# Performance work log

Measured on AMD Instinct MI355X. Metric: run time of the kernel, lower is better.

## Reference

```python
import jax, jax.numpy as jnp
import numpy as np

WS = 9
PAD = WS // 2  # 4


def _unfold(x, H, W):
    # x: [N,C,H,W] -> [N,C,81,H,W], reflect-padded 9x9 windows,
    # tap order (row-major over kernel) matching torch F.unfold.
    xp = jnp.pad(x, ((0, 0), (0, 0), (PAD, PAD), (PAD, PAD)), mode='reflect')
    return jnp.stack(
        [xp[:, :, i:i + H, j:j + W] for i in range(WS) for j in range(WS)],
        axis=2,
    )


def _bilinear_align_corners(x, H, W):
    # torch F.interpolate(mode='bilinear', align_corners=True)
    N, C, h, w = x.shape
    ys = jnp.linspace(0.0, h - 1.0, H)
    xs = jnp.linspace(0.0, w - 1.0, W)
    y0 = jnp.floor(ys).astype(jnp.int32)
    x0 = jnp.floor(xs).astype(jnp.int32)
    y1 = jnp.minimum(y0 + 1, h - 1)
    x1 = jnp.minimum(x0 + 1, w - 1)
    wy = (ys - y0)[:, None]   # [H,1]
    wx = (xs - x0)[None, :]   # [1,W]
    g = lambda yi, xi: x[:, :, yi, :][:, :, :, xi]
    top = g(y0, x0) * (1.0 - wx) + g(y0, x1) * wx
    bot = g(y1, x0) * (1.0 - wx) + g(y1, x1) * wx
    return top * (1.0 - wy) + bot * wy


def setup_inputs() -> dict:
    key = jax.random.key(0)
    ks = jax.random.split(key, 6)
    N, H, W = 4, 128, 128
    return {
        'delta': jax.random.normal(ks[0], (N, 64, H, W), jnp.float32),
        'out': jax.random.normal(ks[1], (N, 2, H // 2, W // 2), jnp.float32),
        'ab_logits': jax.random.normal(ks[2], (N, 81, H * W), jnp.float32),
        'w1': jax.random.normal(ks[3], (16, 64), jnp.float32) * 0.125,
        'b1': jnp.zeros((16,), jnp.float32),
        'w2': jax.random.normal(ks[4], (16, 64), jnp.float32) * 0.125,
        'b2': jnp.zeros((16,), jnp.float32),
        'gamma_d': jnp.ones((), jnp.float32),
        'gamma_s': jnp.ones((), jnp.float32),
    }


def reference(delta, out, ab_logits, w1, b1, w2, b2, gamma_d, gamma_s):
    N, C, H, W = delta.shape
    # 1x1 convs
    f1 = jnp.einsum('nchw,oc->nohw', delta, w1) + b1[None, :, None, None]
    f2 = jnp.einsum('nchw,oc->nohw', delta, w2) + b2[None, :, None, None]
    # windowed squared-distance correlation
    f2_unf = _unfold(f2, H, W).reshape(N, 16, WS * WS, H * W)
    d_center = f1.reshape(N, 16, 1, H * W)
    delta_logits = -jnp.sum((d_center - f2_unf) ** 2, axis=1)  # [N,81,HW]
    attn = jax.nn.softmax(gamma_d * delta_logits + gamma_s * ab_logits, axis=1)
    # weighted local aggregation of (detached, upsampled) out
    out_up = _bilinear_align_corners(jax.lax.stop_gradient(out), H, W)
    out_unf = _unfold(out_up, H, W).reshape(N, 2, WS * WS, H * W)
    out_refine = jnp.sum(out_unf * attn[:, None], axis=2)  # [N,2,HW]
    return out_refine.reshape(N, 2, H, W)
```

## Files before the change

### kernel.cpp

```cpp
#include <hip/hip_runtime.h>

#define HW   16384
#define NPIX 65536

typedef _Float16 f16x2 __attribute__((ext_vector_type(2)));

#if __has_builtin(__builtin_amdgcn_fdot2)
#define DOT2(a, b, c) __builtin_amdgcn_fdot2((a), (b), (c), false)
#else
__device__ __forceinline__ float dot2_fb(f16x2 a, f16x2 b, float c) {
    return fmaf((float)a.x, (float)b.x, fmaf((float)a.y, (float)b.y, c));
}
#define DOT2(a, b, c) dot2_fb((a), (b), (c))
#endif

#if __has_builtin(__builtin_amdgcn_exp2f)
#define EXP2F(x) __builtin_amdgcn_exp2f(x)
#else
#define EXP2F(x) exp2f(x)
#endif

__device__ __forceinline__ unsigned packh2(float a, float b) {
    f16x2 h; h.x = (_Float16)a; h.y = (_Float16)b;
    return __builtin_bit_cast(unsigned, h);
}
__device__ __forceinline__ f16x2 bch(unsigned u) {
    return __builtin_bit_cast(f16x2, u);
}

__global__ __launch_bounds__(256) void pass1_kernel(
    const float* __restrict__ delta, const float* __restrict__ outlo,
    const float* __restrict__ w1, const float* __restrict__ b1,
    const float* __restrict__ w2, const float* __restrict__ b2,
    uint4* __restrict__ f1p4, uint4* __restrict__ f2p4, float2* __restrict__ recp)
{
    const int g = blockIdx.x * 256 + threadIdx.x;
    const int n = g >> 14;
    const int p = g & (HW - 1);

    float acc1[16], acc2[16];
#pragma unroll
    for (int o = 0; o < 16; ++o) { acc1[o] = b1[o]; acc2[o] = b2[o]; }

    const float* db = delta + (size_t)n * 64 * HW + p;
#pragma unroll
    for (int cc = 0; cc < 4; ++cc) {
        float d[16];
#pragma unroll
        for (int j = 0; j < 16; ++j) d[j] = db[(cc * 16 + j) * HW];
#pragma unroll
        for (int o = 0; o < 16; ++o) {
            const float* w1r = w1 + o * 64 + cc * 16;
            const float* w2r = w2 + o * 64 + cc * 16;
#pragma unroll
            for (int j = 0; j < 16; ++j) {
                acc1[o] = fmaf(w1r[j], d[j], acc1[o]);
                acc2[o] = fmaf(w2r[j], d[j], acc2[o]);
            }
        }
    }

    float f2sq = 0.f;
#pragma unroll
    for (int o = 0; o < 16; ++o) f2sq = fmaf(acc2[o], acc2[o], f2sq);

    uint4 q;
    q.x = packh2(acc1[0], acc1[1]);  q.y = packh2(acc1[2], acc1[3]);
    q.z = packh2(acc1[4], acc1[5]);  q.w = packh2(acc1[6], acc1[7]);
    f1p4[g] = q;
    q.x = packh2(acc1[8], acc1[9]);  q.y = packh2(acc1[10], acc1[11]);
    q.z = packh2(acc1[12], acc1[13]);q.w = packh2(acc1[14], acc1[15]);
    f1p4[NPIX + g] = q;
    q.x = packh2(acc2[0], acc2[1]);  q.y = packh2(acc2[2], acc2[3]);
    q.z = packh2(acc2[4], acc2[5]);  q.w = packh2(acc2[6], acc2[7]);
    f2p4[g] = q;
    q.x = packh2(acc2[8], acc2[9]);  q.y = packh2(acc2[10], acc2[11]);
    q.z = packh2(acc2[12], acc2[13]);q.w = packh2(acc2[14], acc2[15]);
    f2p4[NPIX + g] = q;

    const int y = p >> 7, x = p & 127;
    const float ys = (float)(y * 63) / 127.0f;
    const float xs = (float)(x * 63) / 127.0f;
    const int iy0 = (int)ys, ix0 = (int)xs;
    const float fy = ys - (float)iy0, fx = xs - (float)ix0;
    const int iy1 = min(iy0 + 1, 63), ix1 = min(ix0 + 1, 63);
    const float* ob = outlo + n * 2 * 4096;
    float o01[2];
#pragma unroll
    for (int cc = 0; cc < 2; ++cc) {
        const float* oc = ob + cc * 4096;
        const float v00 = oc[iy0*64+ix0], v01 = oc[iy0*64+ix1];
        const float v10 = oc[iy1*64+ix0], v11 = oc[iy1*64+ix1];
        const float top = v00 + fx * (v01 - v00);
        const float bot = v10 + fx * (v11 - v10);
        o01[cc] = top + fy * (bot - top);
    }
    float2 rc;
    rc.x = __builtin_bit_cast(float, packh2(o01[0], o01[1]));
    rc.y = f2sq;
    recp[g] = rc;
}

__global__ __launch_bounds__(128) void pass2_kernel(
    const uint4* __restrict__ f1p4, const uint4* __restrict__ f2p4,
    const float2* __restrict__ recp, const float* __restrict__ ab,
    const float* __restrict__ gdp, const float* __restrict__ gsp,
    float* __restrict__ outp)
{
    __shared__ unsigned sh[24 * 25 * 12];

    const int t = threadIdx.x;
    const int n = blockIdx.z;
    const int bx = blockIdx.x * 16, by = blockIdx.y * 16;

#pragma unroll
    for (int s = 0; s < 5; ++s) {
        const int idx = t + s * 128;
        if (idx < 576) {
            const int hy = idx / 24, hx = idx - hy * 24;
            int gy = by - 4 + hy; gy = gy < 0 ? -gy : (gy > 127 ? 254 - gy : gy);
            int gx = bx - 4 + hx; gx = gx < 0 ? -gx : (gx > 127 ? 254 - gx : gx);
            const int g = n * HW + gy * 128 + gx;
            const uint4  q0 = f2p4[g];
            const uint4  q1 = f2p4[NPIX + g];
            const float2 rc = recp[g];
            const int b = (hy * 25 + hx) * 12;
            *(uint4*)&sh[b]     = q0;
            *(uint4*)&sh[b + 4] = q1;
            *(float2*)&sh[b + 8] = rc;
        }
    }
    __syncthreads();

    const float gd = gdp[0], gs = gsp[0];
    const float L2E = 1.44269504088896f;
    const int tx2 = t & 7, ty = t >> 3;
    const int x0 = bx + tx2 * 2, y = by + ty;
    const int p0 = y * 128 + x0;
    const int g0 = n * HW + p0;

    f16x2 f1a[8], f1b[8];
    {
        const uint4 A0 = f1p4[g0],     A1 = f1p4[NPIX + g0];
        const uint4 B0 = f1p4[g0 + 1], B1 = f1p4[NPIX + g0 + 1];
        f1a[0]=bch(A0.x); f1a[1]=bch(A0.y); f1a[2]=bch(A0.z); f1a[3]=bch(A0.w);
        f1a[4]=bch(A1.x); f1a[5]=bch(A1.y); f1a[6]=bch(A1.z); f1a[7]=bch(A1.w);
        f1b[0]=bch(B0.x); f1b[1]=bch(B0.y); f1b[2]=bch(B0.z); f1b[3]=bch(B0.w);
        f1b[4]=bch(B1.x); f1b[5]=bch(B1.y); f1b[6]=bch(B1.z); f1b[7]=bch(B1.w);
    }
    float f1sqa = 0.f, f1sqb = 0.f;
#pragma unroll
    for (int k = 0; k < 8; ++k) {
        f1sqa = DOT2(f1a[k], f1a[k], f1sqa);
        f1sqb = DOT2(f1b[k], f1b[k], f1sqb);
    }
    const float g2  = 2.0f * gd * L2E;
    const float mg  = -gd * L2E;
    const float gsl = gs * L2E;
    const float c0a = mg * f1sqa;
    const float c0b = mg * f1sqb;

    const float2* abp = (const float2*)ab + (size_t)n * 81 * (HW / 2) + (p0 >> 1);

    float2 cur[9], nxt[9];
#pragma unroll
    for (int j = 0; j < 9; ++j) cur[j] = abp[(size_t)j * (HW / 2)];

    float s0 = 0.f, x00 = 0.f, x01 = 0.f;
    float s1 = 0.f, x10 = 0.f, x11 = 0.f;

    for (int dy = 0; dy < 9; ++dy) {
        const int nr = (dy < 8) ? dy + 1 : 8;
#pragma unroll
        for (int j = 0; j < 9; ++j) nxt[j] = abp[(size_t)(nr * 9 + j) * (HW / 2)];

        const int rowb = ((ty + dy) * 25 + tx2 * 2) * 12;
#pragma unroll
        for (int dxc = 0; dxc < 10; ++dxc) {
            const int b = rowb + dxc * 12;
            const uint4  q0 = *(const uint4*)&sh[b];
            const uint4  q1 = *(const uint4*)&sh[b + 4];
            const float2 rc = *(const float2*)&sh[b + 8];
            f16x2 f2v[8];
            f2v[0]=bch(q0.x); f2v[1]=bch(q0.y); f2v[2]=bch(q0.z); f2v[3]=bch(q0.w);
            f2v[4]=bch(q1.x); f2v[5]=bch(q1.y); f2v[6]=bch(q1.z); f2v[7]=bch(q1.w);
            const f16x2 oh = bch(__builtin_bit_cast(unsigned, rc.x));
            const float o0f = (float)oh.x, o1f = (float)oh.y;
            const float f2s = rc.y;
            if (dxc <= 8) {
                float dt = 0.f;
#pragma unroll
                for (int k = 0; k < 8; ++k) dt = DOT2(f1a[k], f2v[k], dt);
                float e = fmaf(g2, dt, c0a);
                e = fmaf(mg, f2s, e);
                e = fmaf(gsl, cur[dxc].x, e);
                const float w = EXP2F(e);
                s0 += w; x00 = fmaf(w, o0f, x00); x01 = fmaf(w, o1f, x01);
            }
            if (dxc >= 1) {
                float dt = 0.f;
#pragma unroll
                for (int k = 0; k < 8; ++k) dt = DOT2(f1b[k], f2v[k], dt);
                float e = fmaf(g2, dt, c0b);
                e = fmaf(mg, f2s, e);
                e = fmaf(gsl, cur[dxc - 1].y, e);
                const float w = EXP2F(e);
                s1 += w; x10 = fmaf(w, o0f, x10); x11 = fmaf(w, o1f, x11);
            }
        }
#pragma unroll
        for (int j = 0; j < 9; ++j) cur[j] = nxt[j];
    }

    const float i0 = 1.0f / s0, i1 = 1.0f / s1;
    float2* o0p = (float2*)(outp + (size_t)(n * 2 + 0) * HW + p0);
    float2* o1p = (float2*)(outp + (size_t)(n * 2 + 1) * HW + p0);
    *o0p = make_float2(x00 * i0, x10 * i1);
    *o1p = make_float2(x01 * i0, x11 * i1);
}

extern "C" void kernel_launch(void* const* d_in, const int* in_sizes, int n_in,
                              void* d_out, int out_size, void* d_ws, size_t ws_size,
                              hipStream_t stream) {
    const float* delta = (const float*)d_in[0];
    const float* outlo = (const float*)d_in[1];
    const float* ab    = (const float*)d_in[2];
    const float* w1    = (const float*)d_in[3];
    const float* b1    = (const float*)d_in[4];
    const float* w2    = (const float*)d_in[5];
    const float* b2    = (const float*)d_in[6];
    const float* gd    = (const float*)d_in[7];
    const float* gs    = (const float*)d_in[8];
    float* outp = (float*)d_out;

    uint4*  f1p4 = (uint4*)d_ws;
    uint4*  f2p4 = f1p4 + (size_t)2 * NPIX;
    float2* recp = (float2*)(f2p4 + (size_t)2 * NPIX);

    pass1_kernel<<<dim3(256), dim3(256), 0, stream>>>(delta, outlo, w1, b1, w2, b2,
                                                      f1p4, f2p4, recp);
    pass2_kernel<<<dim3(8, 8, 4), dim3(128), 0, stream>>>(f1p4, f2p4, recp, ab,
                                                          gd, gs, outp);
}
```

Before: 116.6 us.

## Split pass1 by conv and pass2 window rows across waves with LDS reduction

Pass1 now launches two blocks per pixel group, one for each 1x1 conv, which doubles parallelism but reads delta twice. Pass2 switches to 8x16 tiles with 256 threads, where each wave handles a subset of window rows for two vertically adjacent pixels. Partial softmax sums are reduced through shared memory. The aim is more waves for the 256-CU GPU and coalesced per-pixel ab loads, at the cost of extra LDS traffic and a second barrier.

```diff
diff --git a/kernel.cpp b/kernel.cpp
--- a/kernel.cpp
+++ b/kernel.cpp
@@ -34,115 +34,111 @@
     const float* __restrict__ w2, const float* __restrict__ b2,
     uint4* __restrict__ f1p4, uint4* __restrict__ f2p4, float2* __restrict__ recp)
 {
+    const int m = blockIdx.y;
     const int g = blockIdx.x * 256 + threadIdx.x;
     const int n = g >> 14;
     const int p = g & (HW - 1);
 
-    float acc1[16], acc2[16];
-#pragma unroll
-    for (int o = 0; o < 16; ++o) { acc1[o] = b1[o]; acc2[o] = b2[o]; }
-
+    const float* __restrict__ wm = m ? w2 : w1;
+    const float* __restrict__ bm = m ? b2 : b1;
+
+    float d[64];
     const float* db = delta + (size_t)n * 64 * HW + p;
 #pragma unroll
-    for (int cc = 0; cc < 4; ++cc) {
-        float d[16];
-#pragma unroll
-        for (int j = 0; j < 16; ++j) d[j] = db[(cc * 16 + j) * HW];
-#pragma unroll
-        for (int o = 0; o < 16; ++o) {
-            const float* w1r = w1 + o * 64 + cc * 16;
-            const float* w2r = w2 + o * 64 + cc * 16;
-#pragma unroll
-            for (int j = 0; j < 16; ++j) {
-                acc1[o] = fmaf(w1r[j], d[j], acc1[o]);
-                acc2[o] = fmaf(w2r[j], d[j], acc2[o]);
-            }
-        }
-    }
-
-    float f2sq = 0.f;
-#pragma unroll
-    for (int o = 0; o < 16; ++o) f2sq = fmaf(acc2[o], acc2[o], f2sq);
-
+    for (int c = 0; c < 64; ++c) d[c] = db[(size_t)c * HW];
+
+    float acc[16];
+#pragma unroll
+    for (int o = 0; o < 16; ++o) {
+        float a = bm[o];
+        const float* wr = wm + o * 64;
+#pragma unroll
+        for (int c = 0; c < 64; ++c) a = fmaf(wr[c], d[c], a);
+        acc[o] = a;
+    }
+
+    uint4* dst = m ? f2p4 : f1p4;
     uint4 q;
-    q.x = packh2(acc1[0], acc1[1]);  q.y = packh2(acc1[2], acc1[3]);
-    q.z = packh2(acc1[4], acc1[5]);  q.w = packh2(acc1[6], acc1[7]);
-    f1p4[g] = q;
-    q.x = packh2(acc1[8], acc1[9]);  q.y = packh2(acc1[10], acc1[11]);
-    q.z = packh2(acc1[12], acc1[13]);q.w = packh2(acc1[14], acc1[15]);
-    f1p4[NPIX + g] = q;
-    q.x = packh2(acc2[0], acc2[1]);  q.y = packh2(acc2[2], acc2[3]);
-    q.z = packh2(acc2[4], acc2[5]);  q.w = packh2(acc2[6], acc2[7]);
-    f2p4[g] = q;
-    q.x = packh2(acc2[8], acc2[9]);  q.y = packh2(acc2[10], acc2[11]);
-    q.z = packh2(acc2[12], acc2[13]);q.w = packh2(acc2[14], acc2[15]);
-    f2p4[NPIX + g] = q;
-
-    const int y = p >> 7, x = p & 127;
-    const float ys = (float)(y * 63) / 127.0f;
-    const float xs = (float)(x * 63) / 127.0f;
-    const int iy0 = (int)ys, ix0 = (int)xs;
-    const float fy = ys - (float)iy0, fx = xs - (float)ix0;
-    const int iy1 = min(iy0 + 1, 63), ix1 = min(ix0 + 1, 63);
-    const float* ob = outlo + n * 2 * 4096;
-    float o01[2];
-#pragma unroll
-    for (int cc = 0; cc < 2; ++cc) {
-        const float* oc = ob + cc * 4096;
-        const float v00 = oc[iy0*64+ix0], v01 = oc[iy0*64+ix1];
-        const float v10 = oc[iy1*64+ix0], v11 = oc[iy1*64+ix1];
-        const float top = v00 + fx * (v01 - v00);
-        const float bot = v10 + fx * (v11 - v10);
-        o01[cc] = top + fy * (bot - top);
-    }
-    float2 rc;
-    rc.x = __builtin_bit_cast(float, packh2(o01[0], o01[1]));
-    rc.y = f2sq;
-    recp[g] = rc;
-}
-
-__global__ __launch_bounds__(128) void pass2_kernel(
+    q.x = packh2(acc[0], acc[1]);   q.y = packh2(acc[2], acc[3]);
+    q.z = packh2(acc[4], acc[5]);   q.w = packh2(acc[6], acc[7]);
+    dst[g] = q;
+    q.x = packh2(acc[8], acc[9]);   q.y = packh2(acc[10], acc[11]);
+    q.z = packh2(acc[12], acc[13]); q.w = packh2(acc[14], acc[15]);
+    dst[NPIX + g] = q;
+
+    if (m) {
+        float f2sq = 0.f;
+#pragma unroll
+        for (int o = 0; o < 16; ++o) f2sq = fmaf(acc[o], acc[o], f2sq);
+
+        const int y = p >> 7, x = p & 127;
+        const float ys = (float)(y * 63) / 127.0f;
+        const float xs = (float)(x * 63) / 127.0f;
+        const int iy0 = (int)ys, ix0 = (int)xs;
+        const float fy = ys - (float)iy0, fx = xs - (float)ix0;
+        const int iy1 = min(iy0 + 1, 63), ix1 = min(ix0 + 1, 63);
+        const float* ob = outlo + n * 2 * 4096;
+        float o01[2];
+#pragma unroll
+        for (int cc = 0; cc < 2; ++cc) {
+            const float* oc = ob + cc * 4096;
+            const float v00 = oc[iy0*64+ix0], v01 = oc[iy0*64+ix1];
+            const float v10 = oc[iy1*64+ix0], v11 = oc[iy1*64+ix1];
+            const float top = v00 + fx * (v01 - v00);
+            const float bot = v10 + fx * (v11 - v10);
+            o01[cc] = top + fy * (bot - top);
+        }
+        float2 rc;
+        rc.x = __builtin_bit_cast(float, packh2(o01[0], o01[1]));
+        rc.y = f2sq;
+        recp[g] = rc;
+    }
+}
+
+__global__ __launch_bounds__(256) void pass2_kernel(
     const uint4* __restrict__ f1p4, const uint4* __restrict__ f2p4,
     const float2* __restrict__ recp, const float* __restrict__ ab,
     const float* __restrict__ gdp, const float* __restrict__ gsp,
     float* __restrict__ outp)
 {
-    __shared__ unsigned sh[24 * 25 * 12];
+    __shared__ uint4  shA[384];
+    __shared__ uint4  shB[384];
+    __shared__ float2 shC[384];
+    __shared__ float  shP[6 * 4 * 64];
 
     const int t = threadIdx.x;
     const int n = blockIdx.z;
-    const int bx = blockIdx.x * 16, by = blockIdx.y * 16;
-
-#pragma unroll
-    for (int s = 0; s < 5; ++s) {
-        const int idx = t + s * 128;
-        if (idx < 576) {
+    const int bx = blockIdx.x * 16, by = blockIdx.y * 8;
+
+#pragma unroll
+    for (int s = 0; s < 2; ++s) {
+        const int idx = t + s * 256;
+        if (idx < 384) {
             const int hy = idx / 24, hx = idx - hy * 24;
             int gy = by - 4 + hy; gy = gy < 0 ? -gy : (gy > 127 ? 254 - gy : gy);
             int gx = bx - 4 + hx; gx = gx < 0 ? -gx : (gx > 127 ? 254 - gx : gx);
-            const int g = n * HW + gy * 128 + gx;
-            const uint4  q0 = f2p4[g];
-            const uint4  q1 = f2p4[NPIX + g];
-            const float2 rc = recp[g];
-            const int b = (hy * 25 + hx) * 12;
-            *(uint4*)&sh[b]     = q0;
-            *(uint4*)&sh[b + 4] = q1;
-            *(float2*)&sh[b + 8] = rc;
+            const int gg = n * HW + gy * 128 + gx;
+            shA[idx] = f2p4[gg];
+            shB[idx] = f2p4[NPIX + gg];
+            shC[idx] = recp[gg];
         }
     }
     __syncthreads();
 
     const float gd = gdp[0], gs = gsp[0];
     const float L2E = 1.44269504088896f;
-    const int tx2 = t & 7, ty = t >> 3;
-    const int x0 = bx + tx2 * 2, y = by + ty;
-    const int p0 = y * 128 + x0;
+    const float g2 = 2.0f * gd * L2E, mg = -gd * L2E, gsl = gs * L2E;
+
+    const int wh = t >> 6;
+    const int l  = t & 63;
+    const int px = l & 15, pyr = l >> 4;
+    const int p0 = (by + pyr * 2) * 128 + bx + px;
     const int g0 = n * HW + p0;
 
     f16x2 f1a[8], f1b[8];
     {
-        const uint4 A0 = f1p4[g0],     A1 = f1p4[NPIX + g0];
-        const uint4 B0 = f1p4[g0 + 1], B1 = f1p4[NPIX + g0 + 1];
+        const uint4 A0 = f1p4[g0],       A1 = f1p4[NPIX + g0];
+        const uint4 B0 = f1p4[g0 + 128], B1 = f1p4[NPIX + g0 + 128];
         f1a[0]=bch(A0.x); f1a[1]=bch(A0.y); f1a[2]=bch(A0.z); f1a[3]=bch(A0.w);
         f1a[4]=bch(A1.x); f1a[5]=bch(A1.y); f1a[6]=bch(A1.z); f1a[7]=bch(A1.w);
         f1b[0]=bch(B0.x); f1b[1]=bch(B0.y); f1b[2]=bch(B0.z); f1b[3]=bch(B0.w);
@@ -154,69 +150,93 @@
         f1sqa = DOT2(f1a[k], f1a[k], f1sqa);
         f1sqb = DOT2(f1b[k], f1b[k], f1sqb);
     }
-    const float g2  = 2.0f * gd * L2E;
-    const float mg  = -gd * L2E;
-    const float gsl = gs * L2E;
     const float c0a = mg * f1sqa;
     const float c0b = mg * f1sqb;
 
-    const float2* abp = (const float2*)ab + (size_t)n * 81 * (HW / 2) + (p0 >> 1);
-
-    float2 cur[9], nxt[9];
-#pragma unroll
-    for (int j = 0; j < 9; ++j) cur[j] = abp[(size_t)j * (HW / 2)];
-
     float s0 = 0.f, x00 = 0.f, x01 = 0.f;
     float s1 = 0.f, x10 = 0.f, x11 = 0.f;
 
-    for (int dy = 0; dy < 9; ++dy) {
-        const int nr = (dy < 8) ? dy + 1 : 8;
-#pragma unroll
-        for (int j = 0; j < 9; ++j) nxt[j] = abp[(size_t)(nr * 9 + j) * (HW / 2)];
-
-        const int rowb = ((ty + dy) * 25 + tx2 * 2) * 12;
-#pragma unroll
-        for (int dxc = 0; dxc < 10; ++dxc) {
-            const int b = rowb + dxc * 12;
-            const uint4  q0 = *(const uint4*)&sh[b];
-            const uint4  q1 = *(const uint4*)&sh[b + 4];
-            const float2 rc = *(const float2*)&sh[b + 8];
-            f16x2 f2v[8];
-            f2v[0]=bch(q0.x); f2v[1]=bch(q0.y); f2v[2]=bch(q0.z); f2v[3]=bch(q0.w);
-            f2v[4]=bch(q1.x); f2v[5]=bch(q1.y); f2v[6]=bch(q1.z); f2v[7]=bch(q1.w);
+    const float* abn = ab + (size_t)n * 81 * HW;
+    const int nrows = (wh < 2) ? 3 : 2;
+
+    for (int r = 0; r < nrows; ++r) {
+        const int dyc = wh + r * 4;
+        const bool has0 = (dyc <= 8);
+        const bool has1 = (dyc >= 1);
+        float a0v[9], a1v[9];
+        if (has0) {
+            const float* a0p = abn + (size_t)(dyc * 9) * HW + p0;
+#pragma unroll
+            for (int j = 0; j < 9; ++j) a0v[j] = a0p[(size_t)j * HW];
+        }
+        if (has1) {
+            const float* a1p = abn + (size_t)((dyc - 1) * 9) * HW + p0 + 128;
+#pragma unroll
+            for (int j = 0; j < 9; ++j) a1v[j] = a1p[(size_t)j * HW];
+        }
+        const int rib = (pyr * 2 + dyc) * 24 + px;
+#pragma unroll
+        for (int j = 0; j < 9; ++j) {
+            const uint4  q0 = shA[rib + j];
+            const uint4  q1 = shB[rib + j];
+            const float2 rc = shC[rib + j];
+            f16x2 v0 = bch(q0.x), v1 = bch(q0.y), v2 = bch(q0.z), v3 = bch(q0.w);
+            f16x2 v4 = bch(q1.x), v5 = bch(q1.y), v6 = bch(q1.z), v7 = bch(q1.w);
             const f16x2 oh = bch(__builtin_bit_cast(unsigned, rc.x));
             const float o0f = (float)oh.x, o1f = (float)oh.y;
             const float f2s = rc.y;
-            if (dxc <= 8) {
-                float dt = 0.f;
-#pragma unroll
-                for (int k = 0; k < 8; ++k) dt = DOT2(f1a[k], f2v[k], dt);
+            if (has0) {
+                float dt = DOT2(f1a[0], v0, 0.f);
+                dt = DOT2(f1a[1], v1, dt); dt = DOT2(f1a[2], v2, dt);
+                dt = DOT2(f1a[3], v3, dt); dt = DOT2(f1a[4], v4, dt);
+                dt = DOT2(f1a[5], v5, dt); dt = DOT2(f1a[6], v6, dt);
+                dt = DOT2(f1a[7], v7, dt);
                 float e = fmaf(g2, dt, c0a);
                 e = fmaf(mg, f2s, e);
-                e = fmaf(gsl, cur[dxc].x, e);
+                e = fmaf(gsl, a0v[j], e);
                 const float w = EXP2F(e);
                 s0 += w; x00 = fmaf(w, o0f, x00); x01 = fmaf(w, o1f, x01);
             }
-            if (dxc >= 1) {
-                float dt = 0.f;
-#pragma unroll
-                for (int k = 0; k < 8; ++k) dt = DOT2(f1b[k], f2v[k], dt);
+            if (has1) {
+                float dt = DOT2(f1b[0], v0, 0.f);
+                dt = DOT2(f1b[1], v1, dt); dt = DOT2(f1b[2], v2, dt);
+                dt = DOT2(f1b[3], v3, dt); dt = DOT2(f1b[4], v4, dt);
+                dt = DOT2(f1b[5], v5, dt); dt = DOT2(f1b[6], v6, dt);
+                dt = DOT2(f1b[7], v7, dt);
                 float e = fmaf(g2, dt, c0b);
                 e = fmaf(mg, f2s, e);
-                e = fmaf(gsl, cur[dxc - 1].y, e);
+                e = fmaf(gsl, a1v[j], e);
                 const float w = EXP2F(e);
                 s1 += w; x10 = fmaf(w, o0f, x10); x11 = fmaf(w, o1f, x11);
             }
         }
-#pragma unroll
-        for (int j = 0; j < 9; ++j) cur[j] = nxt[j];
-    }
-
-    const float i0 = 1.0f / s0, i1 = 1.0f / s1;
-    float2* o0p = (float2*)(outp + (size_t)(n * 2 + 0) * HW + p0);
-    float2* o1p = (float2*)(outp + (size_t)(n * 2 + 1) * HW + p0);
-    *o0p = make_float2(x00 * i0, x10 * i1);
-    *o1p = make_float2(x01 * i0, x11 * i1);
+    }
+
+    shP[(0 * 4 + wh) * 64 + l] = s0;
+    shP[(1 * 4 + wh) * 64 + l] = x00;
+    shP[(2 * 4 + wh) * 64 + l] = x01;
+    shP[(3 * 4 + wh) * 64 + l] = s1;
+    shP[(4 * 4 + wh) * 64 + l] = x10;
+    shP[(5 * 4 + wh) * 64 + l] = x11;
+    __syncthreads();
+
+    if (t < 64) {
+        float v[6];
+#pragma unroll
+        for (int k = 0; k < 6; ++k) {
+            const float* pp = &shP[k * 256 + t];
+            v[k] = (pp[0] + pp[64]) + (pp[128] + pp[192]);
+        }
+        const int qx = t & 15, qyr = t >> 4;
+        const int pp0 = (by + qyr * 2) * 128 + bx + qx;
+        const float i0 = 1.0f / v[0], i1 = 1.0f / v[3];
+        float* o0 = outp + (size_t)(n * 2 + 0) * HW;
+        float* o1 = outp + (size_t)(n * 2 + 1) * HW;
+        o0[pp0]       = v[1] * i0;
+        o1[pp0]       = v[2] * i0;
+        o0[pp0 + 128] = v[4] * i1;
+        o1[pp0 + 128] = v[5] * i1;
+    }
 }
 
 extern "C" void kernel_launch(void* const* d_in, const int* in_sizes, int n_in,
@@ -237,8 +257,8 @@
     uint4*  f2p4 = f1p4 + (size_t)2 * NPIX;
     float2* recp = (float2*)(f2p4 + (size_t)2 * NPIX);
 
-    pass1_kernel<<<dim3(256), dim3(256), 0, stream>>>(delta, outlo, w1, b1, w2, b2,
-                                                      f1p4, f2p4, recp);
-    pass2_kernel<<<dim3(8, 8, 4), dim3(128), 0, stream>>>(f1p4, f2p4, recp, ab,
-                                                          gd, gs, outp);
-}
+    pass1_kernel<<<dim3(256, 2), dim3(256), 0, stream>>>(delta, outlo, w1, b1, w2, b2,
+                                                         f1p4, f2p4, recp);
+    pass2_kernel<<<dim3(8, 16, 4), dim3(256), 0, stream>>>(f1p4, f2p4, recp, ab,
+                                                           gd, gs, outp);
+}
```

Measured after the change: 112.0 us. 4.0% less time.
